# Kernel optimization log

Measured on AMD Instinct MI355X. Metric: run time of the kernel, lower is better.

## Reference

```python
import jax, jax.numpy as jnp
from jax import lax
import numpy as np

RF = 1024   # receptive field
MGC = 60    # mgc feature size
UPS = 200   # upsample factor
MIX = 10    # num mixtures
FS = 256    # filter size
F = 2       # mgc frames
N = F * UPS
SQRT_HALF = 0.70710678118


def setup_inputs() -> dict:
    key = jax.random.key(0)
    ks = jax.random.split(key, 30)
    g = lambda i, shape, s=0.05: jax.random.normal(ks[i], shape, dtype=jnp.float32) * s
    return dict(
        signal=g(0, (N + RF,), 0.3),
        mgc=g(1, (F, MGC), 1.0),
        cond_w=g(2, (MGC * UPS, MGC)), cond_b=g(3, (MGC * UPS,)),
        l0_win=g(4, (FS, 1, 2)), l0_bin=g(5, (FS,)),
        l0_wg=g(6, (FS, 1, 2)), l0_bg=g(7, (FS,)),
        l0_wr=g(8, (FS, 1, 2)), l0_br=g(9, (FS,)),
        lw_in=g(10, (9, FS, FS, 2)), lb_in=g(11, (9, FS)),
        lw_g=g(12, (9, FS, FS, 2)), lb_g=g(13, (9, FS)),
        lw_r=g(14, (9, FS, FS, 2)), lb_r=g(15, (9, FS)),
        cw_in=g(16, (10, FS, MGC)), cb_in=g(17, (10, FS)),
        cw_g=g(18, (10, FS, MGC)), cb_g=g(19, (10, FS)),
        pre_w=g(20, (256, FS)), pre_b=g(21, (256,)),
        mean_w=g(22, (MIX, 256)), mean_b=g(23, (MIX,)),
        std_w=g(24, (MIX, 256)), std_b=g(25, (MIX,)),
        logit_w=g(26, (MIX, 256)), logit_b=g(27, (MIX,)),
    )


def _cond_conv(x, cond, win, bin_, wg, bg, wr, br, wci, bci, wcg, bcg):
    # x: [N, Cin, L]; cond: [N, MGC] -> out: [N, FS, L//2]
    conv = lambda w, b: lax.conv_general_dilated(
        x, w, window_strides=(2,), padding='VALID',
        dimension_numbers=('NCH', 'OIH', 'NCH')) + b[None, :, None]
    it = jnp.tanh(conv(win, bin_) + (cond @ wci.T + bci)[:, :, None])
    gt = jax.nn.sigmoid(conv(wg, bg) + (cond @ wcg.T + bcg)[:, :, None])
    return (it * gt + conv(wr, br)) * SQRT_HALF


def _forward(signal, mgc, cond_w, cond_b,
             l0_win, l0_bin, l0_wg, l0_bg, l0_wr, l0_br,
             lw_in, lb_in, lw_g, lb_g, lw_r, lb_r,
             cw_in, cb_in, cw_g, cb_g,
             pre_w, pre_b, mean_w, mean_b, std_w, std_b, logit_w, logit_b):
    n = signal.shape[0] - RF
    # sliding windows: [n, 1, RF]
    idx = jnp.arange(n)[:, None] + jnp.arange(RF)[None, :]
    x = signal[idx][:, None, :]
    # conditioning: [F, MGC] -> [F, MGC*UPS] -> [F*UPS, MGC]
    cond = jnp.tanh(mgc @ cond_w.T + cond_b).reshape(-1, MGC)
    # WaveNet stack: 10 stride-2 gated conv layers, L: 1024 -> 1
    x = _cond_conv(x, cond, l0_win, l0_bin, l0_wg, l0_bg, l0_wr, l0_br,
                   cw_in[0], cb_in[0], cw_g[0], cb_g[0])
    for i in range(9):
        x = _cond_conv(x, cond, lw_in[i], lb_in[i], lw_g[i], lb_g[i],
                       lw_r[i], lb_r[i], cw_in[i + 1], cb_in[i + 1],
                       cw_g[i + 1], cb_g[i + 1])
    pre = jax.nn.relu(x[:, :, 0] @ pre_w.T + pre_b)  # [n, 256]
    mean = pre @ mean_w.T + mean_b
    stdev = pre @ std_w.T + std_b
    logits = pre @ logit_w.T + logit_b
    return mean, stdev, logits


def reference(signal, mgc, cond_w, cond_b,
              l0_win, l0_bin, l0_wg, l0_bg, l0_wr, l0_br,
              lw_in, lb_in, lw_g, lb_g, lw_r, lb_r,
              cw_in, cb_in, cw_g, cb_g,
              pre_w, pre_b, mean_w, mean_b, std_w, std_b, logit_w, logit_b):
    return _forward(signal, mgc, cond_w, cond_b,
                    l0_win, l0_bin, l0_wg, l0_bg, l0_wr, l0_br,
                    lw_in, lb_in, lw_g, lb_g, lw_r, lb_r,
                    cw_in, cb_in, cw_g, cb_g,
                    pre_w, pre_b, mean_w, mean_b, std_w, std_b,
                    logit_w, logit_b)
```

## Files before the change

### kernel.cpp

```cpp
#include <hip/hip_runtime.h>

typedef unsigned short u16;
using bf16x8 = __attribute__((ext_vector_type(8))) short;
using f32x4  = __attribute__((ext_vector_type(4))) float;

#define SQRT_HALF 0.70710678118f

__device__ __forceinline__ u16 f2bf(float f) {
    union { float f; unsigned int i; } x; x.f = f;
    unsigned int i = x.i;
    unsigned int r = (i + 0x7FFFu + ((i >> 16) & 1u)) >> 16;
    return (u16)r;
}
__device__ __forceinline__ float bf2f(u16 u) {
    union { unsigned int i; float f; } x; x.i = ((unsigned int)u) << 16; return x.f;
}
__device__ __forceinline__ float sigm(float x) { return 1.0f / (1.0f + __expf(-x)); }
__device__ __forceinline__ float tanh_f(float x) {
    float cx = fminf(fmaxf(x, -12.f), 12.f);
    float e = __expf(2.f * cx);
    return (e - 1.f) / (e + 1.f);
}

__global__ void cond_kernel(const float* __restrict__ mgc, const float* __restrict__ cond_w,
                            const float* __restrict__ cond_b, float* __restrict__ cond2) {
    int j = blockIdx.x * 256 + threadIdx.x;
    if (j >= 24000) return;
    int f = j / 12000, jj = j % 12000;
    float s = cond_b[jj];
    const float* wrow = cond_w + (size_t)jj * 60;
    const float* mrow = mgc + f * 60;
    for (int c = 0; c < 60; ++c) s += mrow[c] * wrow[c];
    float v = tanh_f(s);
    int n = f * 200 + jj / 60, cc = jj % 60;
    cond2[n * 60 + cc] = v;
}

__global__ void condadd_kernel(const float* __restrict__ cond2,
                               const float* __restrict__ cw_in, const float* __restrict__ cb_in,
                               const float* __restrict__ cw_g,  const float* __restrict__ cb_g,
                               const float* __restrict__ l0_bin, const float* __restrict__ lb_in,
                               const float* __restrict__ l0_bg,  const float* __restrict__ lb_g,
                               float* __restrict__ ca_in, float* __restrict__ ca_g) {
    int idx = blockIdx.x * 256 + threadIdx.x;
    if (idx >= 10 * 400 * 256) return;
    int co = idx & 255;
    int n  = (idx >> 8) % 400;
    int l  = idx / (400 * 256);
    float si = cb_in[l * 256 + co] + (l == 0 ? l0_bin[co] : lb_in[(l - 1) * 256 + co]);
    float sg = cb_g [l * 256 + co] + (l == 0 ? l0_bg [co] : lb_g [(l - 1) * 256 + co]);
    const float* cn = cond2 + n * 60;
    const float* wi = cw_in + (size_t)(l * 256 + co) * 60;
    const float* wg = cw_g  + (size_t)(l * 256 + co) * 60;
    for (int c = 0; c < 60; ++c) {
        float cv = cn[c];
        si += cv * wi[c];
        sg += cv * wg[c];
    }
    ca_in[idx] = si;
    ca_g[idx]  = sg;
}

__global__ void wreorder_kernel(const float* __restrict__ lw_in, const float* __restrict__ lw_g,
                                const float* __restrict__ lw_r, u16* __restrict__ Wg) {
    int idx = blockIdx.x * 256 + threadIdx.x;
    if (idx >= 9 * 256 * 512) return;
    int kk = idx & 511;
    int co = (idx >> 9) & 255;
    int l  = idx >> 17;
    int k = kk >> 8, ci = kk & 255;
    size_t src = ((size_t)(l * 256 + co) * 256 + ci) * 2 + k;
    size_t dst = (size_t)l * 3 * 131072 + (size_t)co * 512 + kk;
    Wg[dst]              = f2bf(lw_in[src]);
    Wg[dst + 131072]     = f2bf(lw_g[src]);
    Wg[dst + 2 * 131072] = f2bf(lw_r[src]);
}

__global__ void l0_kernel(const float* __restrict__ signal,
                          const float* __restrict__ l0_win, const float* __restrict__ l0_wg,
                          const float* __restrict__ l0_wr,  const float* __restrict__ l0_br,
                          const float* __restrict__ ca_in0, const float* __restrict__ ca_g0,
                          u16* __restrict__ Y0, int n_start) {
    int b = blockIdx.x;
    int tg = b & 127, n_local = b >> 7;
    int n = n_start + n_local;
    int ci = threadIdx.x;
    float wi0 = l0_win[ci * 2], wi1 = l0_win[ci * 2 + 1];
    float wg0 = l0_wg [ci * 2], wg1 = l0_wg [ci * 2 + 1];
    float wr0 = l0_wr [ci * 2], wr1 = l0_wr [ci * 2 + 1];
    float cain = ca_in0[n * 256 + ci], cag = ca_g0[n * 256 + ci], br = l0_br[ci];
    for (int i = 0; i < 4; ++i) {
        int t = tg * 4 + i;
        float s0 = signal[n + 2 * t];
        float s1 = signal[n + 2 * t + 1];
        float vin = wi0 * s0 + wi1 * s1 + cain;
        float vg  = wg0 * s0 + wg1 * s1 + cag;
        float vr  = wr0 * s0 + wr1 * s1 + br;
        float o = (tanh_f(vin) * sigm(vg) + vr) * SQRT_HALF;
        Y0[((size_t)n_local * 512 + t) * 256 + ci] = f2bf(o);
    }
}

__global__ __launch_bounds__(256, 2) void gemm_layer_kernel(
        const u16* __restrict__ A, const u16* __restrict__ Wg,
        const float* __restrict__ ca_in, const float* __restrict__ ca_g,
        const float* __restrict__ br, u16* __restrict__ Y,
        int M, int lg, int n_start) {
    __shared__ u16 Alds[2][128 * 64];
    __shared__ u16 Blds[2][192 * 64];
    int m0  = blockIdx.x * 128;
    int co0 = blockIdx.y * 64;
    int tid = threadIdx.x;
    int lane = tid & 63, wave = tid >> 6;
    int wm = wave & 1, wc = wave >> 1;
    int q = lane >> 4, r16 = lane & 15;

    const u16* agp[4]; int alof[4];
    #pragma unroll
    for (int i = 0; i < 4; ++i) {
        int chunk = tid + i * 256;
        int row = chunk >> 3, c8 = chunk & 7;
        int m = m0 + row;
        int msafe = m < M ? m : (M - 1);
        agp[i] = A + (size_t)msafe * 512 + c8 * 8;
        alof[i] = row * 64 + ((c8 ^ (row & 7)) * 8);
    }
    const u16* bgp[6]; int blof[6];
    #pragma unroll
    for (int i = 0; i < 6; ++i) {
        int chunk = tid + i * 256;
        int row = chunk >> 3, c8 = chunk & 7;
        int conv = row >> 6, col = row & 63;
        bgp[i] = Wg + ((size_t)conv * 256 + co0 + col) * 512 + c8 * 8;
        blof[i] = row * 64 + ((c8 ^ (row & 7)) * 8);
    }

    uint4 ra[4], rb[6];
    #pragma unroll
    for (int i = 0; i < 4; ++i) ra[i] = *(const uint4*)(agp[i]);
    #pragma unroll
    for (int i = 0; i < 6; ++i) rb[i] = *(const uint4*)(bgp[i]);
    #pragma unroll
    for (int i = 0; i < 4; ++i) *(uint4*)(&Alds[0][alof[i]]) = ra[i];
    #pragma unroll
    for (int i = 0; i < 6; ++i) *(uint4*)(&Blds[0][blof[i]]) = rb[i];
    asm volatile("s_waitcnt lgkmcnt(0)\n\ts_barrier" ::: "memory");

    f32x4 acc[3][4][2] = {};

    for (int kt = 0; kt < 8; ++kt) {
        int cur = kt & 1;
        if (kt < 7) {
            #pragma unroll
            for (int i = 0; i < 4; ++i) ra[i] = *(const uint4*)(agp[i] + (kt + 1) * 64);
            #pragma unroll
            for (int i = 0; i < 6; ++i) rb[i] = *(const uint4*)(bgp[i] + (kt + 1) * 64);
        }
        #pragma unroll
        for (int ks = 0; ks < 2; ++ks) {
            int kc = ks * 4 + q;
            bf16x8 af[4], bfr[3][2];
            #pragma unroll
            for (int ms = 0; ms < 4; ++ms) {
                int row = wm * 64 + ms * 16 + r16;
                af[ms] = *(const bf16x8*)(&Alds[cur][row * 64 + (kc ^ (row & 7)) * 8]);
            }
            #pragma unroll
            for (int cv = 0; cv < 3; ++cv)
                #pragma unroll
                for (int cs = 0; cs < 2; ++cs) {
                    int row = cv * 64 + wc * 32 + cs * 16 + r16;
                    bfr[cv][cs] = *(const bf16x8*)(&Blds[cur][row * 64 + (kc ^ (row & 7)) * 8]);
                }
            #pragma unroll
            for (int cv = 0; cv < 3; ++cv)
                #pragma unroll
                for (int ms = 0; ms < 4; ++ms)
                    #pragma unroll
                    for (int cs = 0; cs < 2; ++cs)
                        acc[cv][ms][cs] = __builtin_amdgcn_mfma_f32_16x16x32_bf16(
                            af[ms], bfr[cv][cs], acc[cv][ms][cs], 0, 0, 0);
        }
        asm volatile("s_barrier" ::: "memory");
        if (kt < 7) {
            #pragma unroll
            for (int i = 0; i < 4; ++i) *(uint4*)(&Alds[cur ^ 1][alof[i]]) = ra[i];
            #pragma unroll
            for (int i = 0; i < 6; ++i) *(uint4*)(&Blds[cur ^ 1][blof[i]]) = rb[i];
        }
        asm volatile("s_waitcnt lgkmcnt(0)\n\ts_barrier" ::: "memory");
    }

    #pragma unroll
    for (int ms = 0; ms < 4; ++ms) {
        #pragma unroll
        for (int reg = 0; reg < 4; ++reg) {
            int m = m0 + wm * 64 + ms * 16 + q * 4 + reg;
            if (m >= M) continue;
            int n = n_start + (m >> lg);
            #pragma unroll
            for (int cs = 0; cs < 2; ++cs) {
                int co = co0 + wc * 32 + cs * 16 + r16;
                float vin = acc[0][ms][cs][reg] + ca_in[n * 256 + co];
                float vg  = acc[1][ms][cs][reg] + ca_g [n * 256 + co];
                float vr  = acc[2][ms][cs][reg] + br[co];
                float o = (tanh_f(vin) * sigm(vg) + vr) * SQRT_HALF;
                Y[(size_t)m * 256 + co] = f2bf(o);
            }
        }
    }
}

__global__ __launch_bounds__(256) void head_kernel(
        const u16* __restrict__ Y9, const float* __restrict__ pre_w, const float* __restrict__ pre_b,
        const float* __restrict__ mean_w, const float* __restrict__ mean_b,
        const float* __restrict__ std_w,  const float* __restrict__ std_b,
        const float* __restrict__ logit_w, const float* __restrict__ logit_b,
        float* __restrict__ out, int n_start) {
    __shared__ float xin[256];
    __shared__ float pre[256];
    int n_local = blockIdx.x;
    int n = n_start + n_local;
    int t = threadIdx.x;
    xin[t] = bf2f(Y9[(size_t)n_local * 256 + t]);
    __syncthreads();
    float s = pre_b[t];
    const float* wrow = pre_w + (size_t)t * 256;
    for (int c = 0; c < 256; ++c) s += xin[c] * wrow[c];
    pre[t] = fmaxf(s, 0.f);
    __syncthreads();
    if (t < 30) {
        int head = t / 10, mix = t % 10;
        const float* w  = head == 0 ? mean_w : (head == 1 ? std_w : logit_w);
        const float* bb = head == 0 ? mean_b : (head == 1 ? std_b : logit_b);
        float s2 = bb[mix];
        const float* wr = w + mix * 256;
        for (int c = 0; c < 256; ++c) s2 += pre[c] * wr[c];
        out[head * 4000 + n * 10 + mix] = s2;
    }
}

extern "C" void kernel_launch(void* const* d_in, const int* in_sizes, int n_in,
                              void* d_out, int out_size, void* d_ws, size_t ws_size,
                              hipStream_t stream) {
    const float* signal  = (const float*)d_in[0];
    const float* mgc     = (const float*)d_in[1];
    const float* cond_w  = (const float*)d_in[2];
    const float* cond_b  = (const float*)d_in[3];
    const float* l0_win  = (const float*)d_in[4];
    const float* l0_bin  = (const float*)d_in[5];
    const float* l0_wg   = (const float*)d_in[6];
    const float* l0_bg   = (const float*)d_in[7];
    const float* l0_wr   = (const float*)d_in[8];
    const float* l0_br   = (const float*)d_in[9];
    const float* lw_in   = (const float*)d_in[10];
    const float* lb_in   = (const float*)d_in[11];
    const float* lw_g    = (const float*)d_in[12];
    const float* lb_g    = (const float*)d_in[13];
    const float* lw_r    = (const float*)d_in[14];
    const float* lb_r    = (const float*)d_in[15];
    const float* cw_in   = (const float*)d_in[16];
    const float* cb_in   = (const float*)d_in[17];
    const float* cw_g    = (const float*)d_in[18];
    const float* cb_g    = (const float*)d_in[19];
    const float* pre_w   = (const float*)d_in[20];
    const float* pre_b   = (const float*)d_in[21];
    const float* mean_w  = (const float*)d_in[22];
    const float* mean_b  = (const float*)d_in[23];
    const float* std_w   = (const float*)d_in[24];
    const float* std_b   = (const float*)d_in[25];
    const float* logit_w = (const float*)d_in[26];
    const float* logit_b = (const float*)d_in[27];
    float* out = (float*)d_out;

    char* p = (char*)d_ws;
    auto alloc = [&](size_t bytes) -> char* {
        char* r = p; p += (bytes + 255) & ~(size_t)255; return r;
    };
    u16*   Wg    = (u16*)alloc(7077888);
    float* ca_in = (float*)alloc(4096000);
    float* ca_g  = (float*)alloc(4096000);
    float* cond2 = (float*)alloc(96000);
    size_t fixedBytes = (size_t)(p - (char*)d_ws);

    int c = 1;
    while (c < 16 && fixedBytes + (104857600ull + 52428800ull) / c + 4096 > ws_size) c <<= 1;
    u16* bufA = (u16*)alloc(104857600ull / c);
    u16* bufB = (u16*)alloc(52428800ull / c);
    int n_count = 400 / c;

    cond_kernel<<<94, 256, 0, stream>>>(mgc, cond_w, cond_b, cond2);
    condadd_kernel<<<4000, 256, 0, stream>>>(cond2, cw_in, cb_in, cw_g, cb_g,
                                             l0_bin, lb_in, l0_bg, lb_g, ca_in, ca_g);
    wreorder_kernel<<<4608, 256, 0, stream>>>(lw_in, lw_g, lw_r, Wg);

    for (int ch = 0; ch < c; ++ch) {
        int n_start = ch * n_count;
        l0_kernel<<<n_count * 128, 256, 0, stream>>>(signal, l0_win, l0_wg, l0_wr, l0_br,
                                                     ca_in, ca_g, bufA, n_start);
        u16* src = bufA;
        u16* dst = bufB;
        for (int layer = 1; layer <= 9; ++layer) {
            int lg = 9 - layer;
            int M = n_count << lg;
            dim3 grid((M + 127) / 128, 4);
            gemm_layer_kernel<<<grid, 256, 0, stream>>>(
                src, Wg + (size_t)(layer - 1) * 3 * 131072,
                ca_in + (size_t)layer * 102400, ca_g + (size_t)layer * 102400,
                lb_r + (layer - 1) * 256, dst, M, lg, n_start);
            u16* tswap = src; src = dst; dst = tswap;
        }
        head_kernel<<<n_count, 256, 0, stream>>>(src, pre_w, pre_b, mean_w, mean_b,
                                                 std_w, std_b, logit_w, logit_b, out, n_start);
    }
}
```

Before: 597.2 us.

## Deepen GEMM global prefetch, drop a barrier, swap grid order, vectorize l0 stores

```diff
diff --git a/kernel.cpp b/kernel.cpp
--- a/kernel.cpp
+++ b/kernel.cpp
@@ -82,23 +82,22 @@
                           const float* __restrict__ ca_in0, const float* __restrict__ ca_g0,
                           u16* __restrict__ Y0, int n_start) {
     int b = blockIdx.x;
-    int tg = b & 127, n_local = b >> 7;
+    int tg = b & 63, n_local = b >> 6;
     int n = n_start + n_local;
-    int ci = threadIdx.x;
-    float wi0 = l0_win[ci * 2], wi1 = l0_win[ci * 2 + 1];
-    float wg0 = l0_wg [ci * 2], wg1 = l0_wg [ci * 2 + 1];
-    float wr0 = l0_wr [ci * 2], wr1 = l0_wr [ci * 2 + 1];
-    float cain = ca_in0[n * 256 + ci], cag = ca_g0[n * 256 + ci], br = l0_br[ci];
-    for (int i = 0; i < 4; ++i) {
-        int t = tg * 4 + i;
-        float s0 = signal[n + 2 * t];
-        float s1 = signal[n + 2 * t + 1];
-        float vin = wi0 * s0 + wi1 * s1 + cain;
-        float vg  = wg0 * s0 + wg1 * s1 + cag;
-        float vr  = wr0 * s0 + wr1 * s1 + br;
-        float o = (tanh_f(vin) * sigm(vg) + vr) * SQRT_HALF;
-        Y0[((size_t)n_local * 512 + t) * 256 + ci] = f2bf(o);
-    }
+    int ci0 = (threadIdx.x & 31) * 8;
+    int t = tg * 8 + (threadIdx.x >> 5);
+    float s0 = signal[n + 2 * t];
+    float s1 = signal[n + 2 * t + 1];
+    u16 ov[8];
+    #pragma unroll
+    for (int j = 0; j < 8; ++j) {
+        int ci = ci0 + j;
+        float vin = l0_win[ci * 2] * s0 + l0_win[ci * 2 + 1] * s1 + ca_in0[n * 256 + ci];
+        float vg  = l0_wg [ci * 2] * s0 + l0_wg [ci * 2 + 1] * s1 + ca_g0 [n * 256 + ci];
+        float vr  = l0_wr [ci * 2] * s0 + l0_wr [ci * 2 + 1] * s1 + l0_br[ci];
+        ov[j] = f2bf((tanh_f(vin) * sigm(vg) + vr) * SQRT_HALF);
+    }
+    *(uint4*)(&Y0[((size_t)n_local * 512 + t) * 256 + ci0]) = *(uint4*)ov;
 }
 
 __global__ __launch_bounds__(256, 2) void gemm_layer_kernel(
@@ -108,8 +107,8 @@
         int M, int lg, int n_start) {
     __shared__ u16 Alds[2][128 * 64];
     __shared__ u16 Blds[2][192 * 64];
-    int m0  = blockIdx.x * 128;
-    int co0 = blockIdx.y * 64;
+    int m0  = blockIdx.y * 128;
+    int co0 = blockIdx.x * 64;
     int tid = threadIdx.x;
     int lane = tid & 63, wave = tid >> 6;
     int wm = wave & 1, wc = wave >> 1;
@@ -135,26 +134,33 @@
         blof[i] = row * 64 + ((c8 ^ (row & 7)) * 8);
     }
 
-    uint4 ra[4], rb[6];
-    #pragma unroll
-    for (int i = 0; i < 4; ++i) ra[i] = *(const uint4*)(agp[i]);
-    #pragma unroll
-    for (int i = 0; i < 6; ++i) rb[i] = *(const uint4*)(bgp[i]);
-    #pragma unroll
-    for (int i = 0; i < 4; ++i) *(uint4*)(&Alds[0][alof[i]]) = ra[i];
-    #pragma unroll
-    for (int i = 0; i < 6; ++i) *(uint4*)(&Blds[0][blof[i]]) = rb[i];
+    uint4 ra[2][4], rb[2][6];
+    #pragma unroll
+    for (int i = 0; i < 4; ++i) ra[0][i] = *(const uint4*)(agp[i]);
+    #pragma unroll
+    for (int i = 0; i < 6; ++i) rb[0][i] = *(const uint4*)(bgp[i]);
+    #pragma unroll
+    for (int i = 0; i < 4; ++i) *(uint4*)(&Alds[0][alof[i]]) = ra[0][i];
+    #pragma unroll
+    for (int i = 0; i < 6; ++i) *(uint4*)(&Blds[0][blof[i]]) = rb[0][i];
+    #pragma unroll
+    for (int i = 0; i < 4; ++i) ra[0][i] = *(const uint4*)(agp[i] + 64);
+    #pragma unroll
+    for (int i = 0; i < 6; ++i) rb[0][i] = *(const uint4*)(bgp[i] + 64);
     asm volatile("s_waitcnt lgkmcnt(0)\n\ts_barrier" ::: "memory");
 
     f32x4 acc[3][4][2] = {};
 
+    #pragma unroll
     for (int kt = 0; kt < 8; ++kt) {
-        int cur = kt & 1;
-        if (kt < 7) {
-            #pragma unroll
-            for (int i = 0; i < 4; ++i) ra[i] = *(const uint4*)(agp[i] + (kt + 1) * 64);
-            #pragma unroll
-            for (int i = 0; i < 6; ++i) rb[i] = *(const uint4*)(bgp[i] + (kt + 1) * 64);
+        const int cur  = kt & 1;
+        const int lset = (kt + 1) & 1;
+        const int wset = kt & 1;
+        if (kt < 6) {
+            #pragma unroll
+            for (int i = 0; i < 4; ++i) ra[lset][i] = *(const uint4*)(agp[i] + (kt + 2) * 64);
+            #pragma unroll
+            for (int i = 0; i < 6; ++i) rb[lset][i] = *(const uint4*)(bgp[i] + (kt + 2) * 64);
         }
         #pragma unroll
         for (int ks = 0; ks < 2; ++ks) {
@@ -181,14 +187,13 @@
                         acc[cv][ms][cs] = __builtin_amdgcn_mfma_f32_16x16x32_bf16(
                             af[ms], bfr[cv][cs], acc[cv][ms][cs], 0, 0, 0);
         }
-        asm volatile("s_barrier" ::: "memory");
         if (kt < 7) {
             #pragma unroll
-            for (int i = 0; i < 4; ++i) *(uint4*)(&Alds[cur ^ 1][alof[i]]) = ra[i];
-            #pragma unroll
-            for (int i = 0; i < 6; ++i) *(uint4*)(&Blds[cur ^ 1][blof[i]]) = rb[i];
-        }
-        asm volatile("s_waitcnt lgkmcnt(0)\n\ts_barrier" ::: "memory");
+            for (int i = 0; i < 4; ++i) *(uint4*)(&Alds[cur ^ 1][alof[i]]) = ra[wset][i];
+            #pragma unroll
+            for (int i = 0; i < 6; ++i) *(uint4*)(&Blds[cur ^ 1][blof[i]]) = rb[wset][i];
+            asm volatile("s_waitcnt lgkmcnt(0)\n\ts_barrier" ::: "memory");
+        }
     }
 
     #pragma unroll
@@ -296,14 +301,14 @@
 
     for (int ch = 0; ch < c; ++ch) {
         int n_start = ch * n_count;
-        l0_kernel<<<n_count * 128, 256, 0, stream>>>(signal, l0_win, l0_wg, l0_wr, l0_br,
-                                                     ca_in, ca_g, bufA, n_start);
+        l0_kernel<<<n_count * 64, 256, 0, stream>>>(signal, l0_win, l0_wg, l0_wr, l0_br,
+                                                    ca_in, ca_g, bufA, n_start);
         u16* src = bufA;
         u16* dst = bufB;
         for (int layer = 1; layer <= 9; ++layer) {
             int lg = 9 - layer;
             int M = n_count << lg;
-            dim3 grid((M + 127) / 128, 4);
+            dim3 grid(4, (M + 127) / 128);
             gemm_layer_kernel<<<grid, 256, 0, stream>>>(
                 src, Wg + (size_t)(layer - 1) * 3 * 131072,
                 ca_in + (size_t)layer * 102400, ca_g + (size_t)layer * 102400,
```

New measurement: 865.5 us. 1.45x slower.
